# Performance work log

Hardware: AMD Instinct MI355X
Metric: run time of the kernel (lower is better)

The kernel has to match this reference:

```python
import jax, jax.numpy as jnp
import numpy as np

T, IN, OUT, R = 8192, 4096, 4096, 64


def setup_inputs() -> dict:
    key = jax.random.key(0)
    ks = jax.random.split(key, 7)
    # signed int4 values in [-8, 8) for activations and (unpacked) weights
    quant_x = jax.random.randint(ks[0], (T, IN), -8, 8, dtype=jnp.int32)
    weight_q = jax.random.randint(ks[1], (OUT, IN), -8, 8, dtype=jnp.int32)
    # positive per-token / per-channel symmetric-quant scales
    scale_x = jax.random.uniform(ks[2], (T,), dtype=jnp.float32) * 0.01 + 1e-4
    weight_scales = jax.random.uniform(ks[3], (OUT,), dtype=jnp.float32) * 0.01 + 1e-4
    outlier_x = jax.random.normal(ks[4], (T, R), dtype=jnp.float32)
    w_outlier = jax.random.normal(ks[5], (OUT, R), dtype=jnp.float32)
    bias = jax.random.normal(ks[6], (OUT,), dtype=jnp.float32)
    return {"quant_x": quant_x, "weight_q": weight_q, "scale_x": scale_x,
            "weight_scales": weight_scales, "outlier_x": outlier_x,
            "w_outlier": w_outlier, "bias": bias}


def reference(quant_x, weight_q, scale_x, weight_scales, outlier_x, w_outlier, bias):
    acc = jnp.matmul(quant_x, weight_q.T)
    # sym_dequant: per-row activation scale * per-column weight scale
    x_out = acc.astype(jnp.float32) * scale_x[:, None] * weight_scales[None, :]
    # outlier low-rank addmm + bias epilogue
    x_out = x_out + jnp.matmul(outlier_x, w_outlier.T) + bias
    return x_out
```

## Files before the change

kernel.cpp:

```cpp
#include <hip/hip_runtime.h>

#define T_DIM 8192
#define IN_DIM 4096
#define OUT_DIM 4096
#define R_DIM 64
#define NKT 64

typedef int i32x4 __attribute__((ext_vector_type(4)));
typedef float f32x4 __attribute__((ext_vector_type(4)));
typedef _Float16 f16x8 __attribute__((ext_vector_type(8)));

__device__ __forceinline__ int pack4(int4 v) {
  return (v.x & 255) | ((v.y & 255) << 8) | ((v.z & 255) << 16) | ((unsigned)v.w << 24);
}

__device__ __forceinline__ void gload16(const void* g, void* l) {
  __builtin_amdgcn_global_load_lds(
      (const __attribute__((address_space(1))) void*)(unsigned long long)g,
      (__attribute__((address_space(3))) void*)(unsigned)(unsigned long long)l,
      16, 0, 0);
}

__global__ void cvt_i8_kernel(const int4* __restrict__ src, int4* __restrict__ dst, int n16) {
  int idx = blockIdx.x * blockDim.x + threadIdx.x;
  int stride = gridDim.x * blockDim.x;
  for (int i = idx; i < n16; i += stride) {
    int4 a = src[4 * i + 0], b = src[4 * i + 1], c = src[4 * i + 2], d = src[4 * i + 3];
    int4 r;
    r.x = pack4(a); r.y = pack4(b); r.z = pack4(c); r.w = pack4(d);
    dst[i] = r;
  }
}

__global__ __launch_bounds__(512, 2)
void w4a4_gemm256(const char* __restrict__ A8, const char* __restrict__ B8,
                  const float* __restrict__ sx, const float* __restrict__ sw,
                  const float* __restrict__ ox, const float* __restrict__ ow,
                  const float* __restrict__ bias, float* __restrict__ out) {
  __shared__ __align__(16) char smem[131072];

  const int bid = blockIdx.x;
  const int swz = (bid & 7) * 64 + (bid >> 3);
  const int tm = swz >> 4, tn = swz & 15;
  const int brow = tm * 256, bcol = tn * 256;

  const int t = threadIdx.x;
  const int w = t >> 6, l = t & 63;
  const int wr = w >> 2, wc = w & 3;
  const int l16 = l & 15, lk = l >> 4;

  const int srow = w * 16 + (l >> 2);
  const int scol = ((l & 3) ^ ((l >> 3) & 3)) << 4;
  const char* aS0 = A8 + (size_t)(brow + srow) * IN_DIM + scol;
  const char* aS1 = aS0 + (size_t)128 * IN_DIM;
  const char* bS0 = B8 + (size_t)(bcol + srow) * IN_DIM + scol;
  const char* bS1 = bS0 + (size_t)128 * IN_DIM;
  char* const stDst = smem + w * 1024;

  const int xorc = (lk ^ ((l16 >> 1) & 3)) << 4;
  const char* aR = smem + (wr * 128 + l16) * 64 + xorc;
  const char* bR = smem + 16384 + (wc * 64 + l16) * 64 + xorc;

  i32x4 acc[8][4];
#pragma unroll
  for (int m = 0; m < 8; ++m)
#pragma unroll
    for (int n = 0; n < 4; ++n) acc[m][n] = (i32x4){0, 0, 0, 0};

  auto stage = [&](int kt) {
    const int k0 = kt << 6;
    char* d = stDst + ((kt & 3) << 15);
    gload16(aS0 + k0, d);
    gload16(aS1 + k0, d + 8192);
    gload16(bS0 + k0, d + 16384);
    gload16(bS1 + k0, d + 24576);
  };

  auto compute = [&](int kt) {
    const int bo = (kt & 3) << 15;
    const char* sa = aR + bo;
    const char* sb = bR + bo;
    i32x4 b0 = *(const i32x4*)(sb);
    i32x4 b1 = *(const i32x4*)(sb + 1024);
    i32x4 b2 = *(const i32x4*)(sb + 2048);
    i32x4 b3 = *(const i32x4*)(sb + 3072);
#pragma unroll
    for (int mh = 0; mh < 4; ++mh) {
      i32x4 a0 = *(const i32x4*)(sa + mh * 2048);
      i32x4 a1 = *(const i32x4*)(sa + mh * 2048 + 1024);
      __builtin_amdgcn_s_setprio(1);
      acc[2 * mh][0] = __builtin_amdgcn_mfma_i32_16x16x64_i8(a0, b0, acc[2 * mh][0], 0, 0, 0);
      acc[2 * mh][1] = __builtin_amdgcn_mfma_i32_16x16x64_i8(a0, b1, acc[2 * mh][1], 0, 0, 0);
      acc[2 * mh][2] = __builtin_amdgcn_mfma_i32_16x16x64_i8(a0, b2, acc[2 * mh][2], 0, 0, 0);
      acc[2 * mh][3] = __builtin_amdgcn_mfma_i32_16x16x64_i8(a0, b3, acc[2 * mh][3], 0, 0, 0);
      acc[2 * mh + 1][0] = __builtin_amdgcn_mfma_i32_16x16x64_i8(a1, b0, acc[2 * mh + 1][0], 0, 0, 0);
      acc[2 * mh + 1][1] = __builtin_amdgcn_mfma_i32_16x16x64_i8(a1, b1, acc[2 * mh + 1][1], 0, 0, 0);
      acc[2 * mh + 1][2] = __builtin_amdgcn_mfma_i32_16x16x64_i8(a1, b2, acc[2 * mh + 1][2], 0, 0, 0);
      acc[2 * mh + 1][3] = __builtin_amdgcn_mfma_i32_16x16x64_i8(a1, b3, acc[2 * mh + 1][3], 0, 0, 0);
      __builtin_amdgcn_s_setprio(0);
    }
  };

  stage(0); stage(1); stage(2);

  for (int kt = 0; kt < NKT - 3; ++kt) {
    asm volatile("s_waitcnt vmcnt(8)" ::: "memory");
    __builtin_amdgcn_s_barrier();
    __builtin_amdgcn_sched_barrier(0);
    stage(kt + 3);
    compute(kt);
  }
  asm volatile("s_waitcnt vmcnt(8)" ::: "memory");
  __builtin_amdgcn_s_barrier();
  __builtin_amdgcn_sched_barrier(0);
  compute(NKT - 3);
  asm volatile("s_waitcnt vmcnt(4)" ::: "memory");
  __builtin_amdgcn_s_barrier();
  __builtin_amdgcn_sched_barrier(0);
  compute(NKT - 2);
  asm volatile("s_waitcnt vmcnt(0)" ::: "memory");
  __builtin_amdgcn_s_barrier();
  __builtin_amdgcn_sched_barrier(0);
  compute(NKT - 1);

  const int orow0 = brow + wr * 128 + (lk << 2);
  const int ocol0 = bcol + wc * 64 + l16;
  float swv[4], bvv[4];
#pragma unroll
  for (int n = 0; n < 4; ++n) { swv[n] = sw[ocol0 + n * 16]; bvv[n] = bias[ocol0 + n * 16]; }

  f32x4 facc[8][4];
#pragma unroll
  for (int m = 0; m < 8; ++m)
#pragma unroll
    for (int r = 0; r < 4; ++r) {
      float sxv = sx[orow0 + m * 16 + r];
#pragma unroll
      for (int n = 0; n < 4; ++n) facc[m][n][r] = (float)acc[m][n][r] * sxv * swv[n];
    }

  __syncthreads();
#pragma unroll
  for (int j = 0; j < 4; ++j) {
    int q = j * 512 + t;
    int row = q >> 3, cd = q & 7, cs = cd ^ (row & 7);
    const float* ga = ox + (size_t)(brow + row) * R_DIM + cs * 8;
    float4 f0 = *(const float4*)ga, f1 = *(const float4*)(ga + 4);
    f16x8 h;
    h[0] = (_Float16)f0.x; h[1] = (_Float16)f0.y; h[2] = (_Float16)f0.z; h[3] = (_Float16)f0.w;
    h[4] = (_Float16)f1.x; h[5] = (_Float16)f1.y; h[6] = (_Float16)f1.z; h[7] = (_Float16)f1.w;
    *(f16x8*)(smem + row * 128 + cd * 16) = h;
    const float* gb = ow + (size_t)(bcol + row) * R_DIM + cs * 8;
    f0 = *(const float4*)gb; f1 = *(const float4*)(gb + 4);
    f16x8 g;
    g[0] = (_Float16)f0.x; g[1] = (_Float16)f0.y; g[2] = (_Float16)f0.z; g[3] = (_Float16)f0.w;
    g[4] = (_Float16)f1.x; g[5] = (_Float16)f1.y; g[6] = (_Float16)f1.z; g[7] = (_Float16)f1.w;
    *(f16x8*)(smem + 32768 + row * 128 + cd * 16) = g;
  }
  __syncthreads();

  const char* qa = smem + (wr * 128 + l16) * 128;
  const char* qb = smem + 32768 + (wc * 64 + l16) * 128;
  const int x7 = l16 & 7;
#pragma unroll
  for (int s = 0; s < 2; ++s) {
    const int ca = ((s * 4 + lk) ^ x7) << 4;
    f16x8 hb[4];
#pragma unroll
    for (int n = 0; n < 4; ++n) hb[n] = *(const f16x8*)(qb + n * 2048 + ca);
#pragma unroll
    for (int m = 0; m < 8; ++m) {
      f16x8 ha = *(const f16x8*)(qa + m * 2048 + ca);
#pragma unroll
      for (int n = 0; n < 4; ++n)
        facc[m][n] = __builtin_amdgcn_mfma_f32_16x16x32_f16(ha, hb[n], facc[m][n], 0, 0, 0);
    }
  }

#pragma unroll
  for (int m = 0; m < 8; ++m)
#pragma unroll
    for (int r = 0; r < 4; ++r) {
      float* po = out + (size_t)(orow0 + m * 16 + r) * OUT_DIM + ocol0;
#pragma unroll
      for (int n = 0; n < 4; ++n) po[n * 16] = facc[m][n][r] + bvv[n];
    }
}

__global__ __launch_bounds__(256)
void w4a4_gemm_fb(const int* __restrict__ A32, const int* __restrict__ B32,
                  const float* __restrict__ sx, const float* __restrict__ sw,
                  const float* __restrict__ ox, const float* __restrict__ ow,
                  const float* __restrict__ bias, float* __restrict__ out) {
  __shared__ __align__(16) unsigned char smem[32768];
  char* sA = (char*)smem;
  char* sB = (char*)smem + 8192;

  const int bid = blockIdx.x;
  const int swzb = (bid & 7) * 256 + (bid >> 3);
  const int tm = swzb >> 5, tn = swzb & 31;
  const int brow = tm * 128, bcol = tn * 128;

  const int t = threadIdx.x;
  const int w = t >> 6, l = t & 63;
  const int wr = w >> 1, wc = w & 1;
  const int l16 = l & 15, lk = l >> 4;
  (void)w;

  i32x4 iacc[4][4];
#pragma unroll
  for (int m = 0; m < 4; ++m)
#pragma unroll
    for (int n = 0; n < 4; ++n) iacc[m][n] = (i32x4){0, 0, 0, 0};

  const int ar = t >> 2;
  const int ac = (t & 3) << 4;
  const int* hA0 = A32 + (size_t)(brow + ar) * IN_DIM + ac;
  const int* hA1 = hA0 + (size_t)64 * IN_DIM;
  const int* hB0 = B32 + (size_t)(bcol + ar) * IN_DIM + ac;
  const int* hB1 = hB0 + (size_t)64 * IN_DIM;

  const char* fragA = sA + (size_t)(wr * 64 + l16) * 64 + lk * 16;
  const char* fragB = sB + (size_t)(wc * 64 + l16) * 64 + lk * 16;

  for (int k0 = 0; k0 < IN_DIM; k0 += 64) {
    const int4* pA0 = (const int4*)(hA0 + k0);
    int4 r0 = {pack4(pA0[0]), pack4(pA0[1]), pack4(pA0[2]), pack4(pA0[3])};
    *(int4*)(sA + t * 16) = r0;
    const int4* pA1 = (const int4*)(hA1 + k0);
    int4 r1 = {pack4(pA1[0]), pack4(pA1[1]), pack4(pA1[2]), pack4(pA1[3])};
    *(int4*)(sA + 4096 + t * 16) = r1;
    const int4* pB0 = (const int4*)(hB0 + k0);
    int4 r2 = {pack4(pB0[0]), pack4(pB0[1]), pack4(pB0[2]), pack4(pB0[3])};
    *(int4*)(sB + t * 16) = r2;
    const int4* pB1 = (const int4*)(hB1 + k0);
    int4 r3 = {pack4(pB1[0]), pack4(pB1[1]), pack4(pB1[2]), pack4(pB1[3])};
    *(int4*)(sB + 4096 + t * 16) = r3;
    __syncthreads();
    i32x4 av[4], bv[4];
#pragma unroll
    for (int m = 0; m < 4; ++m) av[m] = *(const i32x4*)(fragA + m * 1024);
#pragma unroll
    for (int n = 0; n < 4; ++n) bv[n] = *(const i32x4*)(fragB + n * 1024);
#pragma unroll
    for (int m = 0; m < 4; ++m)
#pragma unroll
      for (int n = 0; n < 4; ++n)
        iacc[m][n] = __builtin_amdgcn_mfma_i32_16x16x64_i8(av[m], bv[n], iacc[m][n], 0, 0, 0);
    __syncthreads();
  }

  const int orow = brow + wr * 64 + lk * 4;
  const int ocol = bcol + wc * 64 + l16;
  float swv[4], bvv[4];
#pragma unroll
  for (int n = 0; n < 4; ++n) { swv[n] = sw[ocol + n * 16]; bvv[n] = bias[ocol + n * 16]; }

  f32x4 facc[4][4];
#pragma unroll
  for (int m = 0; m < 4; ++m)
#pragma unroll
    for (int r = 0; r < 4; ++r) {
      float sxv = sx[orow + m * 16 + r];
#pragma unroll
      for (int n = 0; n < 4; ++n) facc[m][n][r] = (float)iacc[m][n][r] * sxv * swv[n];
    }

  _Float16* oA = (_Float16*)smem;
  _Float16* oB = (_Float16*)(smem + 16384);
#pragma unroll
  for (int j = 0; j < 4; ++j) {
    int c = j * 256 + t;
    int rr2 = c >> 3, c8 = (c & 7) << 3;
    const float* gp = ox + (size_t)(brow + rr2) * R_DIM + c8;
    float4 f0 = *(const float4*)gp;
    float4 f1 = *(const float4*)(gp + 4);
    f16x8 h;
    h[0] = (_Float16)f0.x; h[1] = (_Float16)f0.y; h[2] = (_Float16)f0.z; h[3] = (_Float16)f0.w;
    h[4] = (_Float16)f1.x; h[5] = (_Float16)f1.y; h[6] = (_Float16)f1.z; h[7] = (_Float16)f1.w;
    *(f16x8*)((char*)oA + (size_t)c * 16) = h;
    const float* gq = ow + (size_t)(bcol + rr2) * R_DIM + c8;
    f0 = *(const float4*)gq; f1 = *(const float4*)(gq + 4);
    f16x8 g;
    g[0] = (_Float16)f0.x; g[1] = (_Float16)f0.y; g[2] = (_Float16)f0.z; g[3] = (_Float16)f0.w;
    g[4] = (_Float16)f1.x; g[5] = (_Float16)f1.y; g[6] = (_Float16)f1.z; g[7] = (_Float16)f1.w;
    *(f16x8*)((char*)oB + (size_t)c * 16) = g;
  }
  __syncthreads();

  const char* qa = (const char*)oA + (size_t)(wr * 64 + l16) * 128 + lk * 16;
  const char* qb = (const char*)oB + (size_t)(wc * 64 + l16) * 128 + lk * 16;
#pragma unroll
  for (int s = 0; s < 2; ++s) {
    f16x8 ha[4], hb[4];
#pragma unroll
    for (int m = 0; m < 4; ++m) ha[m] = *(const f16x8*)(qa + m * 2048 + s * 64);
#pragma unroll
    for (int n = 0; n < 4; ++n) hb[n] = *(const f16x8*)(qb + n * 2048 + s * 64);
#pragma unroll
    for (int m = 0; m < 4; ++m)
#pragma unroll
      for (int n = 0; n < 4; ++n)
        facc[m][n] = __builtin_amdgcn_mfma_f32_16x16x32_f16(ha[m], hb[n], facc[m][n], 0, 0, 0);
  }

#pragma unroll
  for (int m = 0; m < 4; ++m)
#pragma unroll
    for (int r = 0; r < 4; ++r) {
      float* po = out + (size_t)(orow + m * 16 + r) * OUT_DIM + ocol;
#pragma unroll
      for (int n = 0; n < 4; ++n) po[n * 16] = facc[m][n][r] + bvv[n];
    }
}

extern "C" void kernel_launch(void* const* d_in, const int* in_sizes, int n_in,
                              void* d_out, int out_size, void* d_ws, size_t ws_size,
                              hipStream_t stream) {
  const int*   qx   = (const int*)d_in[0];
  const int*   wq   = (const int*)d_in[1];
  const float* sx   = (const float*)d_in[2];
  const float* sw   = (const float*)d_in[3];
  const float* ox   = (const float*)d_in[4];
  const float* ow   = (const float*)d_in[5];
  const float* bias = (const float*)d_in[6];
  float* out = (float*)d_out;

  const size_t needA = (size_t)T_DIM * IN_DIM;
  const size_t needB = (size_t)OUT_DIM * IN_DIM;

  if (ws_size >= needA + needB) {
    char* a8 = (char*)d_ws;
    char* b8 = a8 + needA;
    cvt_i8_kernel<<<1024, 256, 0, stream>>>((const int4*)qx, (int4*)a8, (int)(needA / 16));
    cvt_i8_kernel<<<1024, 256, 0, stream>>>((const int4*)wq, (int4*)b8, (int)(needB / 16));
    w4a4_gemm256<<<512, 512, 0, stream>>>(a8, b8, sx, sw, ox, ow, bias, out);
  } else {
    w4a4_gemm_fb<<<2048, 256, 0, stream>>>(qx, wq, sx, sw, ox, ow, bias, out);
  }
}
```

Before: 193.4 us.

## Interleave global-to-LDS stage loads with MFMA phases in a four-phase k-tile schedule

```diff
diff --git a/kernel.cpp b/kernel.cpp
--- a/kernel.cpp
+++ b/kernel.cpp
@@ -9,6 +9,8 @@
 typedef int i32x4 __attribute__((ext_vector_type(4)));
 typedef float f32x4 __attribute__((ext_vector_type(4)));
 typedef _Float16 f16x8 __attribute__((ext_vector_type(8)));
+
+template <int V> struct IC { static constexpr int value = V; };
 
 __device__ __forceinline__ int pack4(int4 v) {
   return (v.x & 255) | ((v.y & 255) << 8) | ((v.z & 255) << 16) | ((unsigned)v.w << 24);
@@ -76,52 +78,88 @@
     gload16(bS1 + k0, d + 24576);
   };
 
-  auto compute = [&](int kt) {
+#define MFMA8(p, A0, A1)                                                            \
+  acc[2*(p)][0]   = __builtin_amdgcn_mfma_i32_16x16x64_i8(A0, b0, acc[2*(p)][0],   0, 0, 0); \
+  acc[2*(p)][1]   = __builtin_amdgcn_mfma_i32_16x16x64_i8(A0, b1, acc[2*(p)][1],   0, 0, 0); \
+  acc[2*(p)][2]   = __builtin_amdgcn_mfma_i32_16x16x64_i8(A0, b2, acc[2*(p)][2],   0, 0, 0); \
+  acc[2*(p)][3]   = __builtin_amdgcn_mfma_i32_16x16x64_i8(A0, b3, acc[2*(p)][3],   0, 0, 0); \
+  acc[2*(p)+1][0] = __builtin_amdgcn_mfma_i32_16x16x64_i8(A1, b0, acc[2*(p)+1][0], 0, 0, 0); \
+  acc[2*(p)+1][1] = __builtin_amdgcn_mfma_i32_16x16x64_i8(A1, b1, acc[2*(p)+1][1], 0, 0, 0); \
+  acc[2*(p)+1][2] = __builtin_amdgcn_mfma_i32_16x16x64_i8(A1, b2, acc[2*(p)+1][2], 0, 0, 0); \
+  acc[2*(p)+1][3] = __builtin_amdgcn_mfma_i32_16x16x64_i8(A1, b3, acc[2*(p)+1][3], 0, 0, 0);
+
+#define PHASE_SYNC()                                         \
+  __builtin_amdgcn_s_barrier();                              \
+  __builtin_amdgcn_sched_barrier(0);                         \
+  asm volatile("s_waitcnt lgkmcnt(0)" ::: "memory");         \
+  __builtin_amdgcn_sched_barrier(0);
+
+#define PHASE_CLOSE()                                        \
+  __builtin_amdgcn_s_barrier();                              \
+  __builtin_amdgcn_sched_barrier(0);
+
+  auto ktile = [&](int kt, auto stageC, auto vmC) {
+    constexpr int ST = decltype(stageC)::value;
+    constexpr int VM = decltype(vmC)::value;
     const int bo = (kt & 3) << 15;
     const char* sa = aR + bo;
     const char* sb = bR + bo;
+    const int k3 = (kt + 3) << 6;
+    char* d = stDst + (((kt + 3) & 3) << 15);
+
     i32x4 b0 = *(const i32x4*)(sb);
     i32x4 b1 = *(const i32x4*)(sb + 1024);
     i32x4 b2 = *(const i32x4*)(sb + 2048);
     i32x4 b3 = *(const i32x4*)(sb + 3072);
-#pragma unroll
-    for (int mh = 0; mh < 4; ++mh) {
-      i32x4 a0 = *(const i32x4*)(sa + mh * 2048);
-      i32x4 a1 = *(const i32x4*)(sa + mh * 2048 + 1024);
-      __builtin_amdgcn_s_setprio(1);
-      acc[2 * mh][0] = __builtin_amdgcn_mfma_i32_16x16x64_i8(a0, b0, acc[2 * mh][0], 0, 0, 0);
-      acc[2 * mh][1] = __builtin_amdgcn_mfma_i32_16x16x64_i8(a0, b1, acc[2 * mh][1], 0, 0, 0);
-      acc[2 * mh][2] = __builtin_amdgcn_mfma_i32_16x16x64_i8(a0, b2, acc[2 * mh][2], 0, 0, 0);
-      acc[2 * mh][3] = __builtin_amdgcn_mfma_i32_16x16x64_i8(a0, b3, acc[2 * mh][3], 0, 0, 0);
-      acc[2 * mh + 1][0] = __builtin_amdgcn_mfma_i32_16x16x64_i8(a1, b0, acc[2 * mh + 1][0], 0, 0, 0);
-      acc[2 * mh + 1][1] = __builtin_amdgcn_mfma_i32_16x16x64_i8(a1, b1, acc[2 * mh + 1][1], 0, 0, 0);
-      acc[2 * mh + 1][2] = __builtin_amdgcn_mfma_i32_16x16x64_i8(a1, b2, acc[2 * mh + 1][2], 0, 0, 0);
-      acc[2 * mh + 1][3] = __builtin_amdgcn_mfma_i32_16x16x64_i8(a1, b3, acc[2 * mh + 1][3], 0, 0, 0);
-      __builtin_amdgcn_s_setprio(0);
-    }
+    i32x4 a0 = *(const i32x4*)(sa);
+    i32x4 a1 = *(const i32x4*)(sa + 1024);
+    if constexpr (ST) gload16(aS0 + k3, d);
+    PHASE_SYNC();
+    __builtin_amdgcn_s_setprio(1);
+    MFMA8(0, a0, a1);
+    __builtin_amdgcn_s_setprio(0);
+    PHASE_CLOSE();
+
+    a0 = *(const i32x4*)(sa + 2048);
+    a1 = *(const i32x4*)(sa + 3072);
+    if constexpr (ST) gload16(aS1 + k3, d + 8192);
+    PHASE_SYNC();
+    __builtin_amdgcn_s_setprio(1);
+    MFMA8(1, a0, a1);
+    __builtin_amdgcn_s_setprio(0);
+    PHASE_CLOSE();
+
+    a0 = *(const i32x4*)(sa + 4096);
+    a1 = *(const i32x4*)(sa + 5120);
+    if constexpr (ST) gload16(bS0 + k3, d + 16384);
+    PHASE_SYNC();
+    __builtin_amdgcn_s_setprio(1);
+    MFMA8(2, a0, a1);
+    __builtin_amdgcn_s_setprio(0);
+    PHASE_CLOSE();
+
+    a0 = *(const i32x4*)(sa + 6144);
+    a1 = *(const i32x4*)(sa + 7168);
+    if constexpr (ST) gload16(bS1 + k3, d + 24576);
+    PHASE_SYNC();
+    __builtin_amdgcn_s_setprio(1);
+    MFMA8(3, a0, a1);
+    __builtin_amdgcn_s_setprio(0);
+    if constexpr (VM == 8)      asm volatile("s_waitcnt vmcnt(8)" ::: "memory");
+    else if constexpr (VM == 4) asm volatile("s_waitcnt vmcnt(4)" ::: "memory");
+    else if constexpr (VM == 0) asm volatile("s_waitcnt vmcnt(0)" ::: "memory");
+    PHASE_CLOSE();
   };
 
   stage(0); stage(1); stage(2);
-
-  for (int kt = 0; kt < NKT - 3; ++kt) {
-    asm volatile("s_waitcnt vmcnt(8)" ::: "memory");
-    __builtin_amdgcn_s_barrier();
-    __builtin_amdgcn_sched_barrier(0);
-    stage(kt + 3);
-    compute(kt);
-  }
   asm volatile("s_waitcnt vmcnt(8)" ::: "memory");
   __builtin_amdgcn_s_barrier();
   __builtin_amdgcn_sched_barrier(0);
-  compute(NKT - 3);
-  asm volatile("s_waitcnt vmcnt(4)" ::: "memory");
-  __builtin_amdgcn_s_barrier();
-  __builtin_amdgcn_sched_barrier(0);
-  compute(NKT - 2);
-  asm volatile("s_waitcnt vmcnt(0)" ::: "memory");
-  __builtin_amdgcn_s_barrier();
-  __builtin_amdgcn_sched_barrier(0);
-  compute(NKT - 1);
+
+  for (int kt = 0; kt < NKT - 3; ++kt) ktile(kt, IC<1>{}, IC<8>{});
+  ktile(NKT - 3, IC<0>{}, IC<4>{});
+  ktile(NKT - 2, IC<0>{}, IC<0>{});
+  ktile(NKT - 1, IC<0>{}, IC<-1>{});
 
   const int orow0 = brow + wr * 128 + (lk << 2);
   const int ocol0 = bcol + wc * 64 + l16;
```

Result: no change. 193.5 us (+0.1%).
